# Kernel optimization log

Hardware: AMD Instinct MI355X
Metric: run time of the kernel (lower is better)

## Reference

```python
import jax, jax.numpy as jnp
import numpy as np
from jax import lax

SCALE = 2
PAD = 1


def setup_inputs() -> dict:
    key = jax.random.key(0)
    k1, k2, k3 = jax.random.split(key, 3)
    x = jax.random.normal(k1, (8, 64, 128, 128), dtype=jnp.float32)
    # Conv2d init: uniform(-k, k), k = sqrt(1/(in_c*kh*kw))
    k = float(np.sqrt(1.0 / (64 * 3 * 3)))
    weight = jax.random.uniform(k2, (64, 64, 3, 3), dtype=jnp.float32, minval=-k, maxval=k)
    bias = jax.random.uniform(k3, (64,), dtype=jnp.float32, minval=-k, maxval=k)
    return {"x": x, "weight": weight, "bias": bias}


def reference(x, weight, bias):
    # One-hot matmul upsample == nearest-neighbor repeat along H and W.
    up = jnp.repeat(jnp.repeat(x, SCALE, axis=2), SCALE, axis=3)  # [B,C,2H,2W]
    out = lax.conv_general_dilated(
        up, weight,
        window_strides=(1, 1),
        padding=((PAD, PAD), (PAD, PAD)),
        dimension_numbers=("NCHW", "OIHW", "NCHW"),
    )
    return out + bias[None, :, None, None]
```

## Files before the change

### kernel.cpp

```cpp
#include <hip/hip_runtime.h>

#define NB   8
#define NC   64
#define H    128
#define W    128
#define TILE 16

typedef __attribute__((ext_vector_type(8))) short short8;
typedef __attribute__((ext_vector_type(4))) float float4_t;

static __device__ __forceinline__ unsigned short f2bf(float f) {
    unsigned u = __builtin_bit_cast(unsigned, f);
    u += 0x7fffu + ((u >> 16) & 1u);
    return (unsigned short)(u >> 16);
}

__global__ void prep_weights(const float* __restrict__ w, unsigned short* __restrict__ Aw) {
    int t = blockIdx.x * blockDim.x + threadIdx.x;
    if (t >= NC * NC) return;
    int oc = t >> 6, ic = t & 63;
    const float* wp = w + (oc * NC + ic) * 9;
    float wv[3][3];
#pragma unroll
    for (int kh = 0; kh < 3; ++kh)
#pragma unroll
        for (int kw = 0; kw < 3; ++kw) wv[kh][kw] = wp[kh * 3 + kw];
    float rc[2][2][3];
#pragma unroll
    for (int kw = 0; kw < 3; ++kw) {
        rc[0][0][kw] = wv[0][kw];
        rc[0][1][kw] = wv[1][kw] + wv[2][kw];
        rc[1][0][kw] = wv[0][kw] + wv[1][kw];
        rc[1][1][kw] = wv[2][kw];
    }
    int m = oc >> 4;
    int lane = ((ic >> 3) & 3) * 16 + (oc & 15);
    int jj = ic & 7;
#pragma unroll
    for (int pr = 0; pr < 2; ++pr)
#pragma unroll
        for (int pc = 0; pc < 2; ++pc) {
            int p = pr * 2 + pc;
#pragma unroll
            for (int i = 0; i < 2; ++i)
#pragma unroll
                for (int j = 0; j < 2; ++j) {
                    float v;
                    if (pc == 0) v = (j == 0) ? rc[pr][i][0] : (rc[pr][i][1] + rc[pr][i][2]);
                    else         v = (j == 0) ? (rc[pr][i][0] + rc[pr][i][1]) : rc[pr][i][2];
                    int s = (i * 2 + j) * 2 + (ic >> 5);
                    Aw[((((size_t)(p * 8 + s) * 4 + m) * 64 + lane) * 8) + jj] = f2bf(v);
                }
        }
}

__global__ __launch_bounds__(256) void cvt_x(const float* __restrict__ x,
                                             unsigned* __restrict__ xcl32) {
    __shared__ float t[NC][65];
    const int tid = threadIdx.x;
    const int px0 = blockIdx.x * 64;
    const int b = blockIdx.y;
    const float* xb = x + (size_t)b * NC * H * W + px0;
    {
        const int ic4 = tid >> 6, px = tid & 63;
#pragma unroll
        for (int io = 0; io < 16; ++io) {
            int ic = io * 4 + ic4;
            t[ic][px] = xb[(size_t)ic * (H * W) + px];
        }
    }
    __syncthreads();
    {
        const int icp = tid & 31;
#pragma unroll
        for (int po = 0; po < 8; ++po) {
            int px = po * 8 + (tid >> 5);
            unsigned d = (unsigned)f2bf(t[2 * icp][px]) | ((unsigned)f2bf(t[2 * icp + 1][px]) << 16);
            xcl32[((size_t)b * (H * W) + px0 + px) * 32 + icp] = d;
        }
    }
}

__global__ __launch_bounds__(256, 4) void upconv_mfma(
    const unsigned short* __restrict__ xcl, const unsigned short* __restrict__ Aw,
    const float* __restrict__ bias, float* __restrict__ out) {
    const int tid = threadIdx.x;
    const int wave = tid >> 6, lane = tid & 63;
    const int tcl = lane & 15, khi = lane >> 4;

    const int bx = blockIdx.x;
    const int b = bx & 7, tile = bx >> 3;
    const int tx = tile & 7, ty = tile >> 3;
    const int r0 = ty * TILE, c0 = tx * TILE;
    const int z = blockIdx.z, pr = z >> 1, ocg = z & 1;
    const bool edge = (tx == 0) | (tx == 7);

    const unsigned short* xb = xcl + (size_t)b * (H * W) * 64;
    const int laneB = tcl * 64 + khi * 8;
    const int rbase = r0 + wave * 4 + pr - 1;

    float4_t acc[2][4][2];
#pragma unroll
    for (int m = 0; m < 2; ++m)
#pragma unroll
        for (int t = 0; t < 4; ++t)
#pragma unroll
            for (int pc = 0; pc < 2; ++pc) acc[m][t][pc] = (float4_t){0.f, 0.f, 0.f, 0.f};

#pragma unroll
    for (int i = 0; i < 2; ++i) {
#pragma unroll
        for (int ich = 0; ich < 2; ++ich) {
            short8 Af[2][2][2];
#pragma unroll
            for (int j = 0; j < 2; ++j)
#pragma unroll
                for (int pc = 0; pc < 2; ++pc)
#pragma unroll
                    for (int m = 0; m < 2; ++m) {
                        int s = (i * 2 + j) * 2 + ich;
                        int p = pr * 2 + pc;
                        Af[j][pc][m] = *(const short8*)(
                            Aw + (((size_t)(p * 8 + s) * 4 + (ocg * 2 + m)) * 64 + lane) * 8);
                    }
#pragma unroll
            for (int t = 0; t < 4; ++t) {
                const int row = rbase + t + i;
                if ((unsigned)row < (unsigned)H) {
                    const unsigned short* rp = xb + (size_t)row * (W * 64);
                    short8 Bs[3];
#pragma unroll
                    for (int sh = 0; sh < 3; ++sh) {
                        if (!edge) {
                            Bs[sh] = *(const short8*)(rp + (c0 - 1 + sh) * 64 + laneB + ich * 32);
                        } else {
                            int gc = c0 - 1 + sh + tcl;
                            int gcc = gc < 0 ? 0 : (gc > W - 1 ? W - 1 : gc);
                            short8 v = *(const short8*)(rp + gcc * 64 + khi * 8 + ich * 32);
                            if ((unsigned)gc >= (unsigned)W) v = (short8)0;
                            Bs[sh] = v;
                        }
                    }
#pragma unroll
                    for (int pc = 0; pc < 2; ++pc)
#pragma unroll
                        for (int j = 0; j < 2; ++j)
#pragma unroll
                            for (int m = 0; m < 2; ++m)
                                acc[m][t][pc] = __builtin_amdgcn_mfma_f32_16x16x32_bf16(
                                    Af[j][pc][m], Bs[pc + j], acc[m][t][pc], 0, 0, 0);
                }
            }
        }
    }

#pragma unroll
    for (int m = 0; m < 2; ++m) {
        const int ocb = (ocg * 2 + m) * 16 + khi * 4;
        const float4_t bv = *(const float4_t*)(bias + ocb);
#pragma unroll
        for (int t = 0; t < 4; ++t) {
            const int orow = 2 * (r0 + wave * 4 + t) + pr;
#pragma unroll
            for (int reg = 0; reg < 4; ++reg) {
                float2 v = make_float2(acc[m][t][0][reg] + bv[reg],
                                       acc[m][t][1][reg] + bv[reg]);
                size_t idx = (((size_t)(b * NC + ocb + reg) * 256 + orow) * 256) + 2 * (c0 + tcl);
                *reinterpret_cast<float2*>(out + idx) = v;
            }
        }
    }
}

extern "C" void kernel_launch(void* const* d_in, const int* in_sizes, int n_in,
                              void* d_out, int out_size, void* d_ws, size_t ws_size,
                              hipStream_t stream) {
    const float* x    = (const float*)d_in[0];
    const float* wgt  = (const float*)d_in[1];
    const float* bias = (const float*)d_in[2];
    float* out = (float*)d_out;
    unsigned short* Aw  = (unsigned short*)d_ws;
    unsigned short* xcl = (unsigned short*)((char*)d_ws + (64 * 64 * 16) * 2);

    prep_weights<<<dim3(16), dim3(256), 0, stream>>>(wgt, Aw);
    cvt_x<<<dim3(256, NB), dim3(256), 0, stream>>>(x, (unsigned*)xcl);
    upconv_mfma<<<dim3(8 * 64, 1, 4), dim3(256), 0, stream>>>(xcl, Aw, bias, out);
}
```

Baseline: 206.6 us.

## Merge prep kernels, prefetch next input row, use nontemporal output stores

Combines the weight-prep and input-conversion kernels into one launch, using an extra grid row for the weight transform. In the MFMA conv kernel, the next row's B fragments are software-prefetched into registers while the current row is computed. Output writes become nontemporal stores, and the occupancy hint drops from 4 to 3 blocks per SM to give more registers. Prefetching adds register pressure and loads clamped rows that are never used, and the extra grid row idles most of its blocks.

Measured after the change: 212.0 us. +2.6%, slower.

```diff
diff --git a/kernel.cpp b/kernel.cpp
--- a/kernel.cpp
+++ b/kernel.cpp
@@ -8,6 +8,7 @@
 
 typedef __attribute__((ext_vector_type(8))) short short8;
 typedef __attribute__((ext_vector_type(4))) float float4_t;
+typedef __attribute__((ext_vector_type(2))) float float2_t;
 
 static __device__ __forceinline__ unsigned short f2bf(float f) {
     unsigned u = __builtin_bit_cast(unsigned, f);
@@ -15,49 +16,52 @@
     return (unsigned short)(u >> 16);
 }
 
-__global__ void prep_weights(const float* __restrict__ w, unsigned short* __restrict__ Aw) {
-    int t = blockIdx.x * blockDim.x + threadIdx.x;
-    if (t >= NC * NC) return;
-    int oc = t >> 6, ic = t & 63;
-    const float* wp = w + (oc * NC + ic) * 9;
-    float wv[3][3];
-#pragma unroll
-    for (int kh = 0; kh < 3; ++kh)
-#pragma unroll
-        for (int kw = 0; kw < 3; ++kw) wv[kh][kw] = wp[kh * 3 + kw];
-    float rc[2][2][3];
-#pragma unroll
-    for (int kw = 0; kw < 3; ++kw) {
-        rc[0][0][kw] = wv[0][kw];
-        rc[0][1][kw] = wv[1][kw] + wv[2][kw];
-        rc[1][0][kw] = wv[0][kw] + wv[1][kw];
-        rc[1][1][kw] = wv[2][kw];
-    }
-    int m = oc >> 4;
-    int lane = ((ic >> 3) & 3) * 16 + (oc & 15);
-    int jj = ic & 7;
-#pragma unroll
-    for (int pr = 0; pr < 2; ++pr)
-#pragma unroll
-        for (int pc = 0; pc < 2; ++pc) {
-            int p = pr * 2 + pc;
-#pragma unroll
-            for (int i = 0; i < 2; ++i)
-#pragma unroll
-                for (int j = 0; j < 2; ++j) {
-                    float v;
-                    if (pc == 0) v = (j == 0) ? rc[pr][i][0] : (rc[pr][i][1] + rc[pr][i][2]);
-                    else         v = (j == 0) ? (rc[pr][i][0] + rc[pr][i][1]) : rc[pr][i][2];
-                    int s = (i * 2 + j) * 2 + (ic >> 5);
-                    Aw[((((size_t)(p * 8 + s) * 4 + m) * 64 + lane) * 8) + jj] = f2bf(v);
-                }
-        }
-}
-
-__global__ __launch_bounds__(256) void cvt_x(const float* __restrict__ x,
-                                             unsigned* __restrict__ xcl32) {
+__global__ __launch_bounds__(256) void prep_and_cvt(
+    const float* __restrict__ x, const float* __restrict__ w,
+    unsigned* __restrict__ xcl32, unsigned short* __restrict__ Aw) {
     __shared__ float t[NC][65];
     const int tid = threadIdx.x;
+
+    if (blockIdx.y == NB) {
+        if (blockIdx.x >= 16) return;
+        int tt = blockIdx.x * 256 + tid;
+        int oc = tt >> 6, ic = tt & 63;
+        const float* wp = w + (oc * NC + ic) * 9;
+        float wv[3][3];
+#pragma unroll
+        for (int kh = 0; kh < 3; ++kh)
+#pragma unroll
+            for (int kw = 0; kw < 3; ++kw) wv[kh][kw] = wp[kh * 3 + kw];
+        float rc[2][2][3];
+#pragma unroll
+        for (int kw = 0; kw < 3; ++kw) {
+            rc[0][0][kw] = wv[0][kw];
+            rc[0][1][kw] = wv[1][kw] + wv[2][kw];
+            rc[1][0][kw] = wv[0][kw] + wv[1][kw];
+            rc[1][1][kw] = wv[2][kw];
+        }
+        int m = oc >> 4;
+        int lane = ((ic >> 3) & 3) * 16 + (oc & 15);
+        int jj = ic & 7;
+#pragma unroll
+        for (int pr = 0; pr < 2; ++pr)
+#pragma unroll
+            for (int pc = 0; pc < 2; ++pc) {
+                int p = pr * 2 + pc;
+#pragma unroll
+                for (int i = 0; i < 2; ++i)
+#pragma unroll
+                    for (int j = 0; j < 2; ++j) {
+                        float v;
+                        if (pc == 0) v = (j == 0) ? rc[pr][i][0] : (rc[pr][i][1] + rc[pr][i][2]);
+                        else         v = (j == 0) ? (rc[pr][i][0] + rc[pr][i][1]) : rc[pr][i][2];
+                        int s = (i * 2 + j) * 2 + (ic >> 5);
+                        Aw[((((size_t)(p * 8 + s) * 4 + m) * 64 + lane) * 8) + jj] = f2bf(v);
+                    }
+            }
+        return;
+    }
+
     const int px0 = blockIdx.x * 64;
     const int b = blockIdx.y;
     const float* xb = x + (size_t)b * NC * H * W + px0;
@@ -81,7 +85,7 @@
     }
 }
 
-__global__ __launch_bounds__(256, 4) void upconv_mfma(
+__global__ __launch_bounds__(256, 3) void upconv_mfma(
     const unsigned short* __restrict__ xcl, const unsigned short* __restrict__ Aw,
     const float* __restrict__ bias, float* __restrict__ out) {
     const int tid = threadIdx.x;
@@ -123,24 +127,33 @@
                         Af[j][pc][m] = *(const short8*)(
                             Aw + (((size_t)(p * 8 + s) * 4 + (ocg * 2 + m)) * 64 + lane) * 8);
                     }
+
+            auto load_row = [&](short8* B, int row) {
+                int vr = row < 0 ? 0 : (row > H - 1 ? H - 1 : row);
+                const unsigned short* rp = xb + (size_t)vr * (W * 64);
+#pragma unroll
+                for (int sh = 0; sh < 3; ++sh) {
+                    if (!edge) {
+                        B[sh] = *(const short8*)(rp + (c0 - 1 + sh) * 64 + laneB + ich * 32);
+                    } else {
+                        int gc = c0 - 1 + sh + tcl;
+                        int gcc = gc < 0 ? 0 : (gc > W - 1 ? W - 1 : gc);
+                        short8 v = *(const short8*)(rp + gcc * 64 + khi * 8 + ich * 32);
+                        if ((unsigned)gc >= (unsigned)W) v = (short8)0;
+                        B[sh] = v;
+                    }
+                }
+            };
+
+            short8 Bs[3];
+            load_row(Bs, rbase + 0 + i);
 #pragma unroll
             for (int t = 0; t < 4; ++t) {
+                short8 Bn[3];
+                if (t < 3) load_row(Bn, rbase + t + 1 + i);
+
                 const int row = rbase + t + i;
                 if ((unsigned)row < (unsigned)H) {
-                    const unsigned short* rp = xb + (size_t)row * (W * 64);
-                    short8 Bs[3];
-#pragma unroll
-                    for (int sh = 0; sh < 3; ++sh) {
-                        if (!edge) {
-                            Bs[sh] = *(const short8*)(rp + (c0 - 1 + sh) * 64 + laneB + ich * 32);
-                        } else {
-                            int gc = c0 - 1 + sh + tcl;
-                            int gcc = gc < 0 ? 0 : (gc > W - 1 ? W - 1 : gc);
-                            short8 v = *(const short8*)(rp + gcc * 64 + khi * 8 + ich * 32);
-                            if ((unsigned)gc >= (unsigned)W) v = (short8)0;
-                            Bs[sh] = v;
-                        }
-                    }
 #pragma unroll
                     for (int pc = 0; pc < 2; ++pc)
 #pragma unroll
@@ -150,6 +163,7 @@
                                 acc[m][t][pc] = __builtin_amdgcn_mfma_f32_16x16x32_bf16(
                                     Af[j][pc][m], Bs[pc + j], acc[m][t][pc], 0, 0, 0);
                 }
+                if (t < 3) { Bs[0] = Bn[0]; Bs[1] = Bn[1]; Bs[2] = Bn[2]; }
             }
         }
     }
@@ -163,10 +177,11 @@
             const int orow = 2 * (r0 + wave * 4 + t) + pr;
 #pragma unroll
             for (int reg = 0; reg < 4; ++reg) {
-                float2 v = make_float2(acc[m][t][0][reg] + bv[reg],
-                                       acc[m][t][1][reg] + bv[reg]);
+                float2_t v;
+                v.x = acc[m][t][0][reg] + bv[reg];
+                v.y = acc[m][t][1][reg] + bv[reg];
                 size_t idx = (((size_t)(b * NC + ocb + reg) * 256 + orow) * 256) + 2 * (c0 + tcl);
-                *reinterpret_cast<float2*>(out + idx) = v;
+                __builtin_nontemporal_store(v, reinterpret_cast<float2_t*>(out + idx));
             }
         }
     }
@@ -182,7 +197,6 @@
     unsigned short* Aw  = (unsigned short*)d_ws;
     unsigned short* xcl = (unsigned short*)((char*)d_ws + (64 * 64 * 16) * 2);
 
-    prep_weights<<<dim3(16), dim3(256), 0, stream>>>(wgt, Aw);
-    cvt_x<<<dim3(256, NB), dim3(256), 0, stream>>>(x, (unsigned*)xcl);
+    prep_and_cvt<<<dim3(256, NB + 1), dim3(256), 0, stream>>>(x, wgt, (unsigned*)xcl, Aw);
     upconv_mfma<<<dim3(8 * 64, 1, 4), dim3(256), 0, stream>>>(xcl, Aw, bias, out);
 }
```
